# Kernel tuning notes

Hardware: AMD Instinct MI355X
Metric: run time of the kernel (lower is better)

## Reference

```python
import jax, jax.numpy as jnp
import numpy as np

# Scalar-only irreps: 8x0e nodes in, 4x0e edge in, 8x0e edge out, 16x0e node out.
N = 50000          # nodes
E = 800000         # edges
MUL_NODE_IN = 8
MUL_EDGE_IN = 4
MUL_Z = 2 * MUL_NODE_IN          # cat([x[i], x[j]]) -> 16
MUL_EDGE_OUT = 8
MUL_NODE_OUT = 16
W_NUMEL = MUL_EDGE_IN * MUL_Z * MUL_EDGE_OUT  # 512 = edge_tp.weight_numel
RAD_IN, RAD_HID = 16, 64         # radial_neurons=[16, 64]


def setup_inputs() -> dict:
    key = jax.random.key(0)
    ks = jax.random.split(key, 7)
    x = jax.random.normal(ks[0], (N, MUL_NODE_IN), dtype=jnp.float32)
    edge_index = jax.random.randint(ks[1], (2, E), 0, N)
    edge_attr = jax.random.normal(ks[2], (E, MUL_EDGE_IN), dtype=jnp.float32)
    edge_len_emb = jax.random.normal(ks[3], (E, RAD_IN), dtype=jnp.float32)
    # radial MLP (e3nn FullyConnectedNet: normalized linear layers, silu)
    w1 = jax.random.normal(ks[4], (RAD_IN, RAD_HID), dtype=jnp.float32)
    w2 = jax.random.normal(ks[5], (RAD_HID, W_NUMEL), dtype=jnp.float32)
    # node_tp internal shared weights: [mul_node_in, mul_edge_out, mul_node_out]
    w_node = jax.random.normal(ks[6], (MUL_NODE_IN, MUL_EDGE_OUT, MUL_NODE_OUT), dtype=jnp.float32)
    return {"x": x, "edge_index": edge_index, "edge_attr": edge_attr,
            "edge_len_emb": edge_len_emb, "w1": w1, "w2": w2, "w_node": w_node}


def reference(x, edge_index, edge_attr, edge_len_emb, w1, w2, w_node):
    i, j = edge_index[0], edge_index[1]
    # radial MLP -> per-edge TP weights (e3nn normalized linears, silu)
    h = jax.nn.silu(edge_len_emb @ w1 / jnp.sqrt(jnp.float32(RAD_IN)))
    w_edge = (h @ w2 / jnp.sqrt(jnp.float32(RAD_HID)))
    w_edge = w_edge.reshape(E, MUL_EDGE_IN, MUL_Z, MUL_EDGE_OUT)
    # gather + concat: z = cat([x[i], x[j]])  [E, 16]
    z = jnp.concatenate([x[i], x[j]], axis=-1)
    # edge_tp: fully-connected scalar TP with path norm 1/sqrt(mul1*mul2)
    edge_out = jnp.einsum('ea,eb,eabk->ek', edge_attr, z, w_edge)
    edge_out = edge_out / jnp.sqrt(jnp.float32(MUL_EDGE_IN * MUL_Z))
    # scatter-sum to destination nodes j
    e_sum = jax.ops.segment_sum(edge_out, j, num_segments=x.shape[0])
    # node_tp: shared internal weights, path norm 1/sqrt(mul1*mul2)
    x_out = jnp.einsum('na,nb,abk->nk', x, e_sum, w_node)
    x_out = x_out / jnp.sqrt(jnp.float32(MUL_NODE_IN * MUL_EDGE_OUT))
    return (x_out, edge_out)
```

## Files before the change

kernel.cpp:

```cpp
#include <hip/hip_runtime.h>


typedef __attribute__((ext_vector_type(8))) short short8;
typedef __attribute__((ext_vector_type(4))) float floatx4;

__device__ inline unsigned short f2bf(float f) {
    union { float f; unsigned u; } v; v.f = f;
    unsigned r = v.u + 0x7FFFu + ((v.u >> 16) & 1u);
    return (unsigned short)(r >> 16);
}
__device__ inline float bf2f(unsigned short u) {
    union { unsigned u; float f; } v; v.u = ((unsigned)u) << 16;
    return v.f;
}

constexpr int TB   = 512;
constexpr int NBLK = 256;

constexpr int W2_LD = 72;
constexpr int HS_LD = 72;
constexpr int ZT_LD = 40;
constexpr int AT_LD = 40;

__global__ __launch_bounds__(TB, 2) void edge_kernel(
    const float* __restrict__ x,
    const int*   __restrict__ ei,
    const float* __restrict__ attr,
    const float* __restrict__ emb,
    const float* __restrict__ w1,
    const float* __restrict__ w2,
    float* __restrict__ edge_out,
    float* __restrict__ e_sum,
    int E)
{
    __shared__ __align__(16) unsigned short s_w2t[512 * W2_LD];
    __shared__ __align__(16) unsigned short s_hsA[8 * 32 * HS_LD];
    __shared__ __align__(16) unsigned short s_ztA[8 * 16 * ZT_LD];
    __shared__ __align__(16) unsigned short s_atA[8 * 4 * AT_LD];
    __shared__ __align__(16) int            s_vjA[8 * 32];

    const int tid  = threadIdx.x;
    const int wave = tid >> 6;
    const int lane = tid & 63;
    const int m16  = lane & 15;
    const int quad = lane >> 4;

    for (int idx = tid; idx < 512 * 64; idx += TB) {
        const int n = idx & 511, k = idx >> 9;
        s_w2t[n * W2_LD + k] = f2bf(w2[k * 512 + n]);
    }
    __syncthreads();

    short8 w1f[4];
    #pragma unroll
    for (int ct = 0; ct < 4; ++ct) {
        short8 f;
        if (quad < 2) {
            #pragma unroll
            for (int j = 0; j < 8; ++j)
                f[j] = (short)f2bf(w1[(quad * 8 + j) * 64 + ct * 16 + m16]);
        } else {
            #pragma unroll
            for (int j = 0; j < 8; ++j) f[j] = 0;
        }
        w1f[ct] = f;
    }

    unsigned short* hsw = s_hsA + wave * 32 * HS_LD;
    unsigned short* ztw = s_ztA + wave * 16 * ZT_LD;
    unsigned short* atw = s_atA + wave * 4 * AT_LD;
    int*            vjw = s_vjA + wave * 32;

    const int wid = blockIdx.x * 8 + wave;
    const int nw  = NBLK * 8;
    const int ntiles = E >> 5;

    for (int tile = wid; tile < ntiles; tile += nw) {
        const int base = tile << 5;

        if (quad < 2) {
            const int mst = quad * 16 + m16;
            const int e   = base + mst;
            const int vj  = ei[E + e];
            const float4 a4  = *(const float4*)(attr + (size_t)e * 4);
            const int vi  = ei[e];
            const float4 xi0 = *(const float4*)(x + (size_t)vi * 8);
            const float4 xi1 = *(const float4*)(x + (size_t)vi * 8 + 4);
            const float4 xj0 = *(const float4*)(x + (size_t)vj * 8);
            const float4 xj1 = *(const float4*)(x + (size_t)vj * 8 + 4);
            ztw[ 0*ZT_LD+mst]=f2bf(xi0.x); ztw[ 1*ZT_LD+mst]=f2bf(xi0.y);
            ztw[ 2*ZT_LD+mst]=f2bf(xi0.z); ztw[ 3*ZT_LD+mst]=f2bf(xi0.w);
            ztw[ 4*ZT_LD+mst]=f2bf(xi1.x); ztw[ 5*ZT_LD+mst]=f2bf(xi1.y);
            ztw[ 6*ZT_LD+mst]=f2bf(xi1.z); ztw[ 7*ZT_LD+mst]=f2bf(xi1.w);
            ztw[ 8*ZT_LD+mst]=f2bf(xj0.x); ztw[ 9*ZT_LD+mst]=f2bf(xj0.y);
            ztw[10*ZT_LD+mst]=f2bf(xj0.z); ztw[11*ZT_LD+mst]=f2bf(xj0.w);
            ztw[12*ZT_LD+mst]=f2bf(xj1.x); ztw[13*ZT_LD+mst]=f2bf(xj1.y);
            ztw[14*ZT_LD+mst]=f2bf(xj1.z); ztw[15*ZT_LD+mst]=f2bf(xj1.w);
            atw[0*AT_LD+mst]=f2bf(a4.x);   atw[1*AT_LD+mst]=f2bf(a4.y);
            atw[2*AT_LD+mst]=f2bf(a4.z);   atw[3*AT_LD+mst]=f2bf(a4.w);
            vjw[mst] = vj;
        }

        short8 a1[2];
        #pragma unroll
        for (int s = 0; s < 2; ++s) {
            short8 f;
            if (quad < 2) {
                const float* ep = emb + (size_t)(base + s * 16 + m16) * 16 + quad * 8;
                const float4 u0 = *(const float4*)ep;
                const float4 u1 = *(const float4*)(ep + 4);
                f[0]=(short)f2bf(u0.x); f[1]=(short)f2bf(u0.y);
                f[2]=(short)f2bf(u0.z); f[3]=(short)f2bf(u0.w);
                f[4]=(short)f2bf(u1.x); f[5]=(short)f2bf(u1.y);
                f[6]=(short)f2bf(u1.z); f[7]=(short)f2bf(u1.w);
            } else {
                #pragma unroll
                for (int j = 0; j < 8; ++j) f[j] = 0;
            }
            a1[s] = f;
        }

        #pragma unroll
        for (int s = 0; s < 2; ++s) {
            #pragma unroll
            for (int ct = 0; ct < 4; ++ct) {
                floatx4 c = {0.f, 0.f, 0.f, 0.f};
                c = __builtin_amdgcn_mfma_f32_16x16x32_bf16(a1[s], w1f[ct], c, 0, 0, 0);
                #pragma unroll
                for (int r = 0; r < 4; ++r) {
                    const float u  = c[r] * 0.25f;
                    const float sv = u / (1.f + __expf(-u)) * (1.0f / 64.0f);
                    hsw[(s * 16 + quad * 4 + r) * HS_LD + ct * 16 + m16] = f2bf(sv);
                }
            }
        }

        short8 a2[2][2];
        #pragma unroll
        for (int s = 0; s < 2; ++s)
            #pragma unroll
            for (int q = 0; q < 2; ++q)
                a2[s][q] = *(const short8*)(hsw + (s * 16 + m16) * HS_LD + q * 32 + quad * 8);

        float eacc[2][4];
        #pragma unroll
        for (int s = 0; s < 2; ++s)
            #pragma unroll
            for (int r = 0; r < 4; ++r) eacc[s][r] = 0.f;

        #pragma unroll 1
        for (int g = 0; g < 4; ++g) {
            float av[2][4];
            #pragma unroll
            for (int s = 0; s < 2; ++s) {
                const ushort4 a4v = *(const ushort4*)(atw + g * AT_LD + s * 16 + quad * 4);
                av[s][0] = bf2f(a4v.x); av[s][1] = bf2f(a4v.y);
                av[s][2] = bf2f(a4v.z); av[s][3] = bf2f(a4v.w);
            }
            #pragma unroll
            for (int tt = 0; tt < 8; ++tt) {
                const int t = g * 8 + tt;
                short8 b2[2];
                b2[0] = *(const short8*)(s_w2t + (16 * t + m16) * W2_LD + quad * 8);
                b2[1] = *(const short8*)(s_w2t + (16 * t + m16) * W2_LD + 32 + quad * 8);
                const int b_idx = (2 * t + (m16 >> 3)) & 15;
                #pragma unroll
                for (int s = 0; s < 2; ++s) {
                    floatx4 c = {0.f, 0.f, 0.f, 0.f};
                    c = __builtin_amdgcn_mfma_f32_16x16x32_bf16(a2[s][0], b2[0], c, 0, 0, 0);
                    c = __builtin_amdgcn_mfma_f32_16x16x32_bf16(a2[s][1], b2[1], c, 0, 0, 0);
                    const ushort4 zv = *(const ushort4*)(ztw + b_idx * ZT_LD + s * 16 + quad * 4);
                    eacc[s][0] += c[0] * (av[s][0] * bf2f(zv.x));
                    eacc[s][1] += c[1] * (av[s][1] * bf2f(zv.y));
                    eacc[s][2] += c[2] * (av[s][2] * bf2f(zv.z));
                    eacc[s][3] += c[3] * (av[s][3] * bf2f(zv.w));
                }
            }
        }

        #pragma unroll
        for (int s = 0; s < 2; ++s)
            #pragma unroll
            for (int r = 0; r < 4; ++r)
                eacc[s][r] += __shfl_xor(eacc[s][r], 8, 64);

        if (m16 < 8) {
            #pragma unroll
            for (int s = 0; s < 2; ++s) {
                const int4 vjq = *(const int4*)(vjw + s * 16 + quad * 4);
                const int vjr[4] = {vjq.x, vjq.y, vjq.z, vjq.w};
                #pragma unroll
                for (int r = 0; r < 4; ++r) {
                    const int e = base + s * 16 + quad * 4 + r;
                    edge_out[(size_t)e * 8 + m16] = eacc[s][r];
                    atomicAdd(e_sum + (size_t)vjr[r] * 8 + m16, eacc[s][r]);
                }
            }
        }
    }
}

__global__ __launch_bounds__(256) void node_kernel(
    const float* __restrict__ x,
    const float* __restrict__ e_sum,
    const float* __restrict__ w_node,
    float* __restrict__ x_out,
    int N)
{
    __shared__ float s_w[8 * 8 * 16];
    for (int idx = threadIdx.x; idx < 1024; idx += 256) s_w[idx] = w_node[idx];
    __syncthreads();

    const int n = blockIdx.x * 256 + threadIdx.x;
    if (n >= N) return;

    float xa[8], eb[8];
    #pragma unroll
    for (int a = 0; a < 8; ++a) xa[a] = x[(size_t)n * 8 + a];
    #pragma unroll
    for (int b = 0; b < 8; ++b) eb[b] = e_sum[(size_t)n * 8 + b];

    float out[16];
    #pragma unroll
    for (int k = 0; k < 16; ++k) out[k] = 0.f;

    const float4* wv = (const float4*)s_w;
    #pragma unroll
    for (int a = 0; a < 8; ++a) {
        #pragma unroll
        for (int b = 0; b < 8; ++b) {
            const float t = xa[a] * eb[b] * 0.125f;
            #pragma unroll
            for (int k4 = 0; k4 < 4; ++k4) {
                const float4 w = wv[(a * 8 + b) * 4 + k4];
                out[k4 * 4 + 0] = fmaf(t, w.x, out[k4 * 4 + 0]);
                out[k4 * 4 + 1] = fmaf(t, w.y, out[k4 * 4 + 1]);
                out[k4 * 4 + 2] = fmaf(t, w.z, out[k4 * 4 + 2]);
                out[k4 * 4 + 3] = fmaf(t, w.w, out[k4 * 4 + 3]);
            }
        }
    }

    float4* xo = (float4*)(x_out + (size_t)n * 16);
    #pragma unroll
    for (int k4 = 0; k4 < 4; ++k4)
        xo[k4] = make_float4(out[k4 * 4 + 0], out[k4 * 4 + 1],
                             out[k4 * 4 + 2], out[k4 * 4 + 3]);
}

extern "C" void kernel_launch(void* const* d_in, const int* in_sizes, int n_in,
                              void* d_out, int out_size, void* d_ws, size_t ws_size,
                              hipStream_t stream) {
    const float* x      = (const float*)d_in[0];
    const int*   ei     = (const int*)d_in[1];
    const float* attr   = (const float*)d_in[2];
    const float* emb    = (const float*)d_in[3];
    const float* w1     = (const float*)d_in[4];
    const float* w2     = (const float*)d_in[5];
    const float* w_node = (const float*)d_in[6];

    const int N = in_sizes[0] / 8;
    const int E = in_sizes[2] / 4;

    float* x_out    = (float*)d_out;
    float* edge_out = (float*)d_out + (size_t)N * 16;
    float* e_sum    = (float*)d_ws;

    hipMemsetAsync(e_sum, 0, (size_t)N * 8 * sizeof(float), stream);

    edge_kernel<<<NBLK, TB, 0, stream>>>(x, ei, attr, emb, w1, w2,
                                         edge_out, e_sum, E);

    node_kernel<<<(N + 255) / 256, 256, 0, stream>>>(x, e_sum, w_node, x_out, N);
}
```

Before: 222.8 us.

## Transpose edge MFMA so edges are columns, keep z/attr in registers

Swaps the MFMA operand roles in the edge tensor-product so the w2 tile is the A operand and the hidden activations are B. Each lane then holds outputs for a single edge, and the per-edge attr*z scale becomes one scalar from registers rather than bf16 values read from shared memory. The w2 staging is re-laid-out to be contiguous per lane, the z/attr/vj shared buffers are dropped, and the block grows to 12 waves with 3 blocks per CU requested. Output is written as float4 stores, and atomics now target contiguous channels per edge. The risks are higher register pressure from the full unroll and the in-register z/attr, and heavier shared memory use from the larger block.

```diff
diff --git a/kernel.cpp b/kernel.cpp
--- a/kernel.cpp
+++ b/kernel.cpp
@@ -9,20 +9,12 @@
     unsigned r = v.u + 0x7FFFu + ((v.u >> 16) & 1u);
     return (unsigned short)(r >> 16);
 }
-__device__ inline float bf2f(unsigned short u) {
-    union { unsigned u; float f; } v; v.u = ((unsigned)u) << 16;
-    return v.f;
-}
-
-constexpr int TB   = 512;
-constexpr int NBLK = 256;
-
-constexpr int W2_LD = 72;
+
+constexpr int TB    = 768;
+constexpr int NBLK  = 256;
 constexpr int HS_LD = 72;
-constexpr int ZT_LD = 40;
-constexpr int AT_LD = 40;
-
-__global__ __launch_bounds__(TB, 2) void edge_kernel(
+
+__global__ __launch_bounds__(TB, 3) void edge_kernel(
     const float* __restrict__ x,
     const int*   __restrict__ ei,
     const float* __restrict__ attr,
@@ -33,114 +25,101 @@
     float* __restrict__ e_sum,
     int E)
 {
-    __shared__ __align__(16) unsigned short s_w2t[512 * W2_LD];
-    __shared__ __align__(16) unsigned short s_hsA[8 * 32 * HS_LD];
-    __shared__ __align__(16) unsigned short s_ztA[8 * 16 * ZT_LD];
-    __shared__ __align__(16) unsigned short s_atA[8 * 4 * AT_LD];
-    __shared__ __align__(16) int            s_vjA[8 * 32];
+    __shared__ __align__(16) unsigned short s_w2n[32768];
+    __shared__ __align__(16) unsigned short s_hsA[12 * 32 * HS_LD];
 
     const int tid  = threadIdx.x;
+    const int lane = tid & 63;
     const int wave = tid >> 6;
-    const int lane = tid & 63;
     const int m16  = lane & 15;
-    const int quad = lane >> 4;
-
-    for (int idx = tid; idx < 512 * 64; idx += TB) {
-        const int n = idx & 511, k = idx >> 9;
-        s_w2t[n * W2_LD + k] = f2bf(w2[k * 512 + n]);
-    }
-    __syncthreads();
+    const int q    = lane >> 4;
+    const int qk   = q & 1;
+    const int par  = q >> 1;
+
+    for (int idx = tid; idx < 32768; idx += TB) {
+        const int j  = idx & 7;
+        const int L  = (idx >> 3) & 63;
+        const int th = idx >> 9;
+        s_w2n[idx] = f2bf(w2[(32 * (th & 1) + 8 * (L >> 4) + j) * 512
+                             + 16 * (th >> 1) + (L & 15)]);
+    }
 
     short8 w1f[4];
     #pragma unroll
     for (int ct = 0; ct < 4; ++ct) {
         short8 f;
-        if (quad < 2) {
-            #pragma unroll
-            for (int j = 0; j < 8; ++j)
-                f[j] = (short)f2bf(w1[(quad * 8 + j) * 64 + ct * 16 + m16]);
-        } else {
-            #pragma unroll
-            for (int j = 0; j < 8; ++j) f[j] = 0;
-        }
+        #pragma unroll
+        for (int j = 0; j < 8; ++j)
+            f[j] = (q < 2) ? (short)f2bf(w1[(8 * q + j) * 64 + 16 * ct + m16])
+                           : (short)0;
         w1f[ct] = f;
     }
+    __syncthreads();
 
     unsigned short* hsw = s_hsA + wave * 32 * HS_LD;
-    unsigned short* ztw = s_ztA + wave * 16 * ZT_LD;
-    unsigned short* atw = s_atA + wave * 4 * AT_LD;
-    int*            vjw = s_vjA + wave * 32;
-
-    const int wid = blockIdx.x * 8 + wave;
-    const int nw  = NBLK * 8;
+
     const int ntiles = E >> 5;
-
-    for (int tile = wid; tile < ntiles; tile += nw) {
+    for (int tile = blockIdx.x * 12 + wave; tile < ntiles; tile += NBLK * 12) {
         const int base = tile << 5;
 
-        if (quad < 2) {
-            const int mst = quad * 16 + m16;
-            const int e   = base + mst;
-            const int vj  = ei[E + e];
-            const float4 a4  = *(const float4*)(attr + (size_t)e * 4);
-            const int vi  = ei[e];
+        int   vja[2];
+        float zsr[2][8];
+        float atr[2][4];
+
+        #pragma unroll
+        for (int s = 0; s < 2; ++s) {
+            const int e  = base + s * 16 + m16;
+            const int vi = ei[e];
+            const int vj = ei[E + e];
+            vja[s] = vj;
+
             const float4 xi0 = *(const float4*)(x + (size_t)vi * 8);
             const float4 xi1 = *(const float4*)(x + (size_t)vi * 8 + 4);
             const float4 xj0 = *(const float4*)(x + (size_t)vj * 8);
             const float4 xj1 = *(const float4*)(x + (size_t)vj * 8 + 4);
-            ztw[ 0*ZT_LD+mst]=f2bf(xi0.x); ztw[ 1*ZT_LD+mst]=f2bf(xi0.y);
-            ztw[ 2*ZT_LD+mst]=f2bf(xi0.z); ztw[ 3*ZT_LD+mst]=f2bf(xi0.w);
-            ztw[ 4*ZT_LD+mst]=f2bf(xi1.x); ztw[ 5*ZT_LD+mst]=f2bf(xi1.y);
-            ztw[ 6*ZT_LD+mst]=f2bf(xi1.z); ztw[ 7*ZT_LD+mst]=f2bf(xi1.w);
-            ztw[ 8*ZT_LD+mst]=f2bf(xj0.x); ztw[ 9*ZT_LD+mst]=f2bf(xj0.y);
-            ztw[10*ZT_LD+mst]=f2bf(xj0.z); ztw[11*ZT_LD+mst]=f2bf(xj0.w);
-            ztw[12*ZT_LD+mst]=f2bf(xj1.x); ztw[13*ZT_LD+mst]=f2bf(xj1.y);
-            ztw[14*ZT_LD+mst]=f2bf(xj1.z); ztw[15*ZT_LD+mst]=f2bf(xj1.w);
-            atw[0*AT_LD+mst]=f2bf(a4.x);   atw[1*AT_LD+mst]=f2bf(a4.y);
-            atw[2*AT_LD+mst]=f2bf(a4.z);   atw[3*AT_LD+mst]=f2bf(a4.w);
-            vjw[mst] = vj;
-        }
-
-        short8 a1[2];
-        #pragma unroll
-        for (int s = 0; s < 2; ++s) {
-            short8 f;
-            if (quad < 2) {
-                const float* ep = emb + (size_t)(base + s * 16 + m16) * 16 + quad * 8;
+            zsr[s][0] = par ? xi0.y : xi0.x;  zsr[s][1] = par ? xi0.w : xi0.z;
+            zsr[s][2] = par ? xi1.y : xi1.x;  zsr[s][3] = par ? xi1.w : xi1.z;
+            zsr[s][4] = par ? xj0.y : xj0.x;  zsr[s][5] = par ? xj0.w : xj0.z;
+            zsr[s][6] = par ? xj1.y : xj1.x;  zsr[s][7] = par ? xj1.w : xj1.z;
+
+            const float4 a4 = *(const float4*)(attr + (size_t)e * 4);
+            atr[s][0] = a4.x; atr[s][1] = a4.y;
+            atr[s][2] = a4.z; atr[s][3] = a4.w;
+
+            short8 a1;
+            if (q < 2) {
+                const float* ep = emb + (size_t)e * 16 + 8 * q;
                 const float4 u0 = *(const float4*)ep;
                 const float4 u1 = *(const float4*)(ep + 4);
-                f[0]=(short)f2bf(u0.x); f[1]=(short)f2bf(u0.y);
-                f[2]=(short)f2bf(u0.z); f[3]=(short)f2bf(u0.w);
-                f[4]=(short)f2bf(u1.x); f[5]=(short)f2bf(u1.y);
-                f[6]=(short)f2bf(u1.z); f[7]=(short)f2bf(u1.w);
+                a1[0]=(short)f2bf(u0.x); a1[1]=(short)f2bf(u0.y);
+                a1[2]=(short)f2bf(u0.z); a1[3]=(short)f2bf(u0.w);
+                a1[4]=(short)f2bf(u1.x); a1[5]=(short)f2bf(u1.y);
+                a1[6]=(short)f2bf(u1.z); a1[7]=(short)f2bf(u1.w);
             } else {
                 #pragma unroll
-                for (int j = 0; j < 8; ++j) f[j] = 0;
-            }
-            a1[s] = f;
-        }
-
-        #pragma unroll
-        for (int s = 0; s < 2; ++s) {
+                for (int j = 0; j < 8; ++j) a1[j] = 0;
+            }
+
             #pragma unroll
             for (int ct = 0; ct < 4; ++ct) {
-                floatx4 c = {0.f, 0.f, 0.f, 0.f};
-                c = __builtin_amdgcn_mfma_f32_16x16x32_bf16(a1[s], w1f[ct], c, 0, 0, 0);
+                floatx4 c0 = {0.f, 0.f, 0.f, 0.f};
+                c0 = __builtin_amdgcn_mfma_f32_16x16x32_bf16(a1, w1f[ct], c0, 0, 0, 0);
                 #pragma unroll
                 for (int r = 0; r < 4; ++r) {
-                    const float u  = c[r] * 0.25f;
+                    const float u  = c0[r] * 0.25f;
                     const float sv = u / (1.f + __expf(-u)) * (1.0f / 64.0f);
-                    hsw[(s * 16 + quad * 4 + r) * HS_LD + ct * 16 + m16] = f2bf(sv);
+                    hsw[(s * 16 + q * 4 + r) * HS_LD + ct * 16 + m16] = f2bf(sv);
                 }
             }
         }
 
-        short8 a2[2][2];
+        short8 hb[2][2];
         #pragma unroll
         for (int s = 0; s < 2; ++s)
             #pragma unroll
-            for (int q = 0; q < 2; ++q)
-                a2[s][q] = *(const short8*)(hsw + (s * 16 + m16) * HS_LD + q * 32 + quad * 8);
+            for (int h = 0; h < 2; ++h)
+                hb[s][h] = *(const short8*)(hsw + (s * 16 + m16) * HS_LD
+                                            + 32 * h + 8 * q);
 
         float eacc[2][4];
         #pragma unroll
@@ -148,32 +127,24 @@
             #pragma unroll
             for (int r = 0; r < 4; ++r) eacc[s][r] = 0.f;
 
-        #pragma unroll 1
+        #pragma unroll
         for (int g = 0; g < 4; ++g) {
-            float av[2][4];
-            #pragma unroll
-            for (int s = 0; s < 2; ++s) {
-                const ushort4 a4v = *(const ushort4*)(atw + g * AT_LD + s * 16 + quad * 4);
-                av[s][0] = bf2f(a4v.x); av[s][1] = bf2f(a4v.y);
-                av[s][2] = bf2f(a4v.z); av[s][3] = bf2f(a4v.w);
-            }
             #pragma unroll
             for (int tt = 0; tt < 8; ++tt) {
                 const int t = g * 8 + tt;
-                short8 b2[2];
-                b2[0] = *(const short8*)(s_w2t + (16 * t + m16) * W2_LD + quad * 8);
-                b2[1] = *(const short8*)(s_w2t + (16 * t + m16) * W2_LD + 32 + quad * 8);
-                const int b_idx = (2 * t + (m16 >> 3)) & 15;
+                const short8 wA0 = *(const short8*)(s_w2n + (t * 2 + 0) * 512 + lane * 8);
+                const short8 wA1 = *(const short8*)(s_w2n + (t * 2 + 1) * 512 + lane * 8);
+                const int bi = t & 7;
                 #pragma unroll
                 for (int s = 0; s < 2; ++s) {
                     floatx4 c = {0.f, 0.f, 0.f, 0.f};
-                    c = __builtin_amdgcn_mfma_f32_16x16x32_bf16(a2[s][0], b2[0], c, 0, 0, 0);
-                    c = __builtin_amdgcn_mfma_f32_16x16x32_bf16(a2[s][1], b2[1], c, 0, 0, 0);
-                    const ushort4 zv = *(const ushort4*)(ztw + b_idx * ZT_LD + s * 16 + quad * 4);
-                    eacc[s][0] += c[0] * (av[s][0] * bf2f(zv.x));
-                    eacc[s][1] += c[1] * (av[s][1] * bf2f(zv.y));
-                    eacc[s][2] += c[2] * (av[s][2] * bf2f(zv.z));
-                    eacc[s][3] += c[3] * (av[s][3] * bf2f(zv.w));
+                    c = __builtin_amdgcn_mfma_f32_16x16x32_bf16(wA0, hb[s][0], c, 0, 0, 0);
+                    c = __builtin_amdgcn_mfma_f32_16x16x32_bf16(wA1, hb[s][1], c, 0, 0, 0);
+                    const float o = atr[s][g] * zsr[s][bi];
+                    eacc[s][0] += c[0] * o;
+                    eacc[s][1] += c[1] * o;
+                    eacc[s][2] += c[2] * o;
+                    eacc[s][3] += c[3] * o;
                 }
             }
         }
@@ -182,19 +153,19 @@
         for (int s = 0; s < 2; ++s)
             #pragma unroll
             for (int r = 0; r < 4; ++r)
-                eacc[s][r] += __shfl_xor(eacc[s][r], 8, 64);
-
-        if (m16 < 8) {
+                eacc[s][r] += __shfl_xor(eacc[s][r], 32);
+
+        if (q < 2) {
             #pragma unroll
             for (int s = 0; s < 2; ++s) {
-                const int4 vjq = *(const int4*)(vjw + s * 16 + quad * 4);
-                const int vjr[4] = {vjq.x, vjq.y, vjq.z, vjq.w};
-                #pragma unroll
-                for (int r = 0; r < 4; ++r) {
-                    const int e = base + s * 16 + quad * 4 + r;
-                    edge_out[(size_t)e * 8 + m16] = eacc[s][r];
-                    atomicAdd(e_sum + (size_t)vjr[r] * 8 + m16, eacc[s][r]);
-                }
+                const int e = base + s * 16 + m16;
+                *(float4*)(edge_out + (size_t)e * 8 + 4 * qk) =
+                    make_float4(eacc[s][0], eacc[s][1], eacc[s][2], eacc[s][3]);
+                float* dst = e_sum + (size_t)vja[s] * 8 + 4 * qk;
+                atomicAdd(dst + 0, eacc[s][0]);
+                atomicAdd(dst + 1, eacc[s][1]);
+                atomicAdd(dst + 2, eacc[s][2]);
+                atomicAdd(dst + 3, eacc[s][3]);
             }
         }
     }
```

Result: slower. 307.6 us (+38.1%).
